# Optimization experiments

Measured on AMD Instinct MI355X. Metric: run time of the kernel, lower is better.

Reference implementation:

```python
import jax, jax.numpy as jnp
import numpy as np

COMMITMENT_COST = 0.25
EMBEDDING_DIM = 64
NUM_EMBEDDINGS = 512
BATCH, SEQ = 64, 4096


def setup_inputs() -> dict:
    key = jax.random.key(0)
    k1, k2, k3 = jax.random.split(key, 3)
    return {
        "inputs": jax.random.normal(k1, (BATCH, SEQ, EMBEDDING_DIM), dtype=jnp.float32),
        "embedding": jax.random.normal(k2, (NUM_EMBEDDINGS, EMBEDDING_DIM), dtype=jnp.float32),
        "ema_cluster_size": jax.random.uniform(k3, (NUM_EMBEDDINGS,), dtype=jnp.float32),
    }


def reference(inputs, embedding, ema_cluster_size):
    # inputs: [B, T, D]; embedding: [K, D]; ema_cluster_size: [K]
    input_shape = inputs.shape
    flat = inputs.reshape(-1, EMBEDDING_DIM)  # [N, D]
    distances = (
        jnp.sum(flat * flat, axis=1, keepdims=True)
        + jnp.sum(embedding * embedding, axis=1)[None, :]
        - 2.0 * (flat @ embedding.T)
    )
    # cluster-size weighting (as in the source module)
    distances = distances * jnp.sqrt(ema_cluster_size)[None, :]
    encoding_indices = jnp.argmin(distances, axis=1)  # [N]
    # one-hot @ codebook == gather
    quantized = embedding[encoding_indices].reshape(input_shape)
    e_latent_loss = jnp.mean((jax.lax.stop_gradient(quantized) - inputs) ** 2)
    loss = COMMITMENT_COST * e_latent_loss
    # straight-through estimator
    quantized_st = inputs + jax.lax.stop_gradient(quantized - inputs)
    return quantized_st, loss, encoding_indices[:, None]
```

## Files before the change

### kernel.cpp

```cpp
#include <hip/hip_runtime.h>
#include <math.h>

#define D 64
#define K 512

typedef __attribute__((ext_vector_type(8))) short short8;
typedef __attribute__((ext_vector_type(4))) float f32x4;

#define WS_E2    256
#define WS_SQ    2304
#define WS_E2SQ  4352
#define WS_TSQ   6400
#define WS_BP    8448
#define WS_WL    139520
#define WS_PART  1188096
#define WS_PART2 1204480

#define KEYMASK 0xFFFFFE00u

__device__ __forceinline__ unsigned short f32_to_bf16_rne(float f)
{
    unsigned int u = __float_as_uint(f);
    unsigned int r = (u + 0x7FFFu + ((u >> 16) & 1u)) >> 16;
    return (unsigned short)r;
}
__device__ __forceinline__ float bf16_to_f32(unsigned short h)
{
    return __uint_as_float(((unsigned int)h) << 16);
}

__device__ __forceinline__ float np_sumsq64(const float* v)
{
#pragma clang fp contract(off)
    float p[64];
#pragma unroll
    for (int i = 0; i < 64; ++i) p[i] = v[i] * v[i];
    float r[8];
#pragma unroll
    for (int j = 0; j < 8; ++j) r[j] = p[j];
#pragma unroll
    for (int b = 8; b < 64; b += 8) {
#pragma unroll
        for (int j = 0; j < 8; ++j) r[j] += p[b + j];
    }
    return ((r[0] + r[1]) + (r[2] + r[3])) + ((r[4] + r[5]) + (r[6] + r[7]));
}

__global__ __launch_bounds__(256) void vq_pack_prep(
    const float* __restrict__ emb,
    const float* __restrict__ cs,
    unsigned short* __restrict__ Bp,
    float* __restrict__ e2,
    float* __restrict__ sq,
    float* __restrict__ e2sq,
    float* __restrict__ tsq,
    int* __restrict__ cnt)
{
    int i = blockIdx.x * blockDim.x + threadIdx.x;
    if (i < 65536) {
        int j    = i & 7;
        int lane = (i >> 3) & 63;
        int kc   = (i >> 9) & 1;
        int ctl  = (i >> 10) & 7;
        int sB   = (i >> 13) & 1;
        int chunk = (i >> 14) & 3;
        int code = chunk * 128 + ctl * 16 + (lane & 15);
        int d    = kc * 32 + (lane >> 4) * 8 + j;
        float v = emb[code * 64 + d];
        unsigned short b0 = f32_to_bf16_rne(v);
        Bp[i] = (sB == 0) ? b0 : f32_to_bf16_rne(v - bf16_to_f32(b0));
    } else if (i < 66048) {
        int k = i - 65536;
        float er[64];
        const float* ek = emb + (size_t)k * D;
#pragma unroll
        for (int d = 0; d < 64; ++d) er[d] = ek[d];
        float e2v = np_sumsq64(er);
        float sqv = (float)sqrt((double)cs[k]);
        e2[k]   = e2v;
        sq[k]   = sqv;
        e2sq[k] = e2v * sqv;
        tsq[k]  = 2.0f * sqv;
    } else if (i == 66048) {
        *cnt = 0;
    }
}

__global__ __launch_bounds__(256) void vq_screen(
    const float* __restrict__ x,
    const float* __restrict__ emb,
    const float* __restrict__ e2sqg,
    const float* __restrict__ tsqg,
    const unsigned short* __restrict__ Bp,
    float* __restrict__ out_q,
    float* __restrict__ out_idx,
    int* __restrict__ wl,
    int* __restrict__ cnt,
    double* __restrict__ partial)
{
    __shared__ unsigned short BpS[16384];
    __shared__ float e2sqs[512];
    __shared__ float tsqs[512];
    __shared__ double ls[4];

    const int wave = threadIdx.x >> 6;
    const int lane = threadIdx.x & 63;
    const int quad = lane >> 4;
    const int n16  = lane & 15;
    const int n0   = blockIdx.x * 128 + wave * 32;

    e2sqs[threadIdx.x]       = e2sqg[threadIdx.x];
    e2sqs[threadIdx.x + 256] = e2sqg[threadIdx.x + 256];
    tsqs[threadIdx.x]        = tsqg[threadIdx.x];
    tsqs[threadIdx.x + 256]  = tsqg[threadIdx.x + 256];

    short8 A0[2][2], A1[2][2];
    float x2h[2][4];
#pragma unroll
    for (int rt = 0; rt < 2; ++rt) {
        float s = 0.0f;
#pragma unroll
        for (int kc = 0; kc < 2; ++kc) {
            const float* src = x + (size_t)(n0 + rt * 16 + n16) * 64
                               + kc * 32 + quad * 8;
            float4 v0 = *(const float4*)(src);
            float4 v1 = *(const float4*)(src + 4);
            float xv[8] = {v0.x, v0.y, v0.z, v0.w, v1.x, v1.y, v1.z, v1.w};
#pragma unroll
            for (int j = 0; j < 8; ++j) {
                float v = xv[j];
                unsigned short b0 = f32_to_bf16_rne(v);
                unsigned short b1 = f32_to_bf16_rne(v - bf16_to_f32(b0));
                A0[rt][kc][j] = (short)b0;
                A1[rt][kc][j] = (short)b1;
                s = fmaf(v, v, s);
            }
        }
        s += __shfl_xor(s, 16, 64);
        s += __shfl_xor(s, 32, 64);
#pragma unroll
        for (int r = 0; r < 4; ++r)
            x2h[rt][r] = 0.5f * __shfl(s, quad * 4 + r, 64);
    }

    unsigned k1[2][4], k2[2][4];
#pragma unroll
    for (int rt = 0; rt < 2; ++rt)
#pragma unroll
        for (int r = 0; r < 4; ++r) { k1[rt][r] = 0xFFFFFFFFu; k2[rt][r] = 0xFFFFFFFFu; }

    for (int chunk = 0; chunk < 4; ++chunk) {
        __syncthreads();
        {
            const float4* src = (const float4*)(Bp + chunk * 16384);
            float4* dst = (float4*)BpS;
#pragma unroll
            for (int it = 0; it < 8; ++it)
                dst[threadIdx.x + it * 256] = src[threadIdx.x + it * 256];
        }
        __syncthreads();

        for (int ctl = 0; ctl < 8; ++ctl) {
            const short8 B00 = *(const short8*)(BpS + (ctl * 2 + 0) * 512 + lane * 8);
            const short8 B01 = *(const short8*)(BpS + (ctl * 2 + 1) * 512 + lane * 8);
            const short8 B10 = *(const short8*)(BpS + ((8 + ctl) * 2 + 0) * 512 + lane * 8);
            const short8 B11 = *(const short8*)(BpS + ((8 + ctl) * 2 + 1) * 512 + lane * 8);

            int c = chunk * 128 + ctl * 16 + n16;
            float e2sqc = e2sqs[c];
            float tsqc  = tsqs[c];

#pragma unroll
            for (int rt = 0; rt < 2; ++rt) {
                f32x4 acc = {0.0f, 0.0f, 0.0f, 0.0f};
                acc = __builtin_amdgcn_mfma_f32_16x16x32_bf16(A0[rt][0], B00, acc, 0, 0, 0);
                acc = __builtin_amdgcn_mfma_f32_16x16x32_bf16(A0[rt][1], B01, acc, 0, 0, 0);
                acc = __builtin_amdgcn_mfma_f32_16x16x32_bf16(A0[rt][0], B10, acc, 0, 0, 0);
                acc = __builtin_amdgcn_mfma_f32_16x16x32_bf16(A0[rt][1], B11, acc, 0, 0, 0);
                acc = __builtin_amdgcn_mfma_f32_16x16x32_bf16(A1[rt][0], B00, acc, 0, 0, 0);
                acc = __builtin_amdgcn_mfma_f32_16x16x32_bf16(A1[rt][1], B01, acc, 0, 0, 0);

#pragma unroll
                for (int r = 0; r < 4; ++r) {
                    float dist = fmaf(x2h[rt][r], tsqc, e2sqc);
                    dist = fmaf(-tsqc, acc[r], dist);
                    dist = fmaxf(dist, 0.0f);
                    unsigned key = (__float_as_uint(dist) & KEYMASK) | (unsigned)c;
                    unsigned a1 = k1[rt][r];
                    unsigned mx = a1 > key ? a1 : key;
                    k1[rt][r] = a1 < key ? a1 : key;
                    k2[rt][r] = k2[rt][r] < mx ? k2[rt][r] : mx;
                }
            }
        }
    }

#pragma unroll
    for (int rt = 0; rt < 2; ++rt)
#pragma unroll
        for (int r = 0; r < 4; ++r) {
            unsigned a1 = k1[rt][r], a2 = k2[rt][r];
#pragma unroll
            for (int w = 1; w < 16; w <<= 1) {
                unsigned o1 = (unsigned)__shfl_xor((int)a1, w, 64);
                unsigned o2 = (unsigned)__shfl_xor((int)a2, w, 64);
                unsigned mx  = a1 > o1 ? a1 : o1;
                a1 = a1 < o1 ? a1 : o1;
                unsigned mn2 = a2 < o2 ? a2 : o2;
                a2 = mn2 < mx ? mn2 : mx;
            }
            k1[rt][r] = a1; k2[rt][r] = a2;
        }

    unsigned pk[2][4];
#pragma unroll
    for (int rt = 0; rt < 2; ++rt)
#pragma unroll
        for (int r = 0; r < 4; ++r) {
            float d1f = __uint_as_float(k1[rt][r] & KEYMASK);
            float d2f = __uint_as_float(k2[rt][r] & KEYMASK);
            int   i1  = (int)(k1[rt][r] & 0x1FFu);
            int   flg = (d2f - d1f) <= (0.01f + 2.0e-4f * d2f);
            pk[rt][r] = (unsigned)i1 | (flg ? 0x8000u : 0u);
            if (n16 == 0) {
                int p = n0 + rt * 16 + quad * 4 + r;
                out_idx[p] = (float)i1;
                if (flg) { int slot = atomicAdd(cnt, 1); wl[slot] = p; }
            }
        }

    int src = (n16 >> 2) * 16 + n16;
    double s = 0.0;
#pragma unroll
    for (int rt = 0; rt < 2; ++rt) {
        unsigned p0 = (unsigned)__shfl((int)pk[rt][0], src, 64);
        unsigned p1 = (unsigned)__shfl((int)pk[rt][1], src, 64);
        unsigned p2 = (unsigned)__shfl((int)pk[rt][2], src, 64);
        unsigned p3 = (unsigned)__shfl((int)pk[rt][3], src, 64);
        int rr = n16 & 3;
        unsigned pm = (rr == 0) ? p0 : (rr == 1) ? p1 : (rr == 2) ? p2 : p3;
        int bim = (int)(pm & 0x1FFu);
        int flg = (int)((pm >> 15) & 1u);
        if (!flg) {
            int prow = n0 + rt * 16 + n16;
#pragma unroll
            for (int kc = 0; kc < 2; ++kc) {
                const float* xs = x   + (size_t)prow * 64 + kc * 32 + quad * 8;
                const float* es = emb + (size_t)bim  * 64 + kc * 32 + quad * 8;
                float4 xv0 = *(const float4*)(xs);
                float4 xv1 = *(const float4*)(xs + 4);
                float4 ev0 = *(const float4*)(es);
                float4 ev1 = *(const float4*)(es + 4);
                float4 o0, o1;
                float t0, t1, t2, t3, t4, t5, t6, t7;
                {
#pragma clang fp contract(off)
                    t0 = ev0.x - xv0.x; o0.x = xv0.x + t0;
                    t1 = ev0.y - xv0.y; o0.y = xv0.y + t1;
                    t2 = ev0.z - xv0.z; o0.z = xv0.z + t2;
                    t3 = ev0.w - xv0.w; o0.w = xv0.w + t3;
                    t4 = ev1.x - xv1.x; o1.x = xv1.x + t4;
                    t5 = ev1.y - xv1.y; o1.y = xv1.y + t5;
                    t6 = ev1.z - xv1.z; o1.z = xv1.z + t6;
                    t7 = ev1.w - xv1.w; o1.w = xv1.w + t7;
                }
                float* od = out_q + (size_t)prow * 64 + kc * 32 + quad * 8;
                *(float4*)(od)     = o0;
                *(float4*)(od + 4) = o1;
                s += (double)t0 * t0 + (double)t1 * t1
                   + (double)t2 * t2 + (double)t3 * t3
                   + (double)t4 * t4 + (double)t5 * t5
                   + (double)t6 * t6 + (double)t7 * t7;
            }
        }
    }

#pragma unroll
    for (int off = 32; off > 0; off >>= 1)
        s += __shfl_down(s, off, 64);
    if (lane == 0) ls[wave] = s;
    __syncthreads();
    if (threadIdx.x == 0)
        partial[blockIdx.x] = ls[0] + ls[1] + ls[2] + ls[3];
}

__global__ __launch_bounds__(256) void vq_exact(
    const float* __restrict__ x,
    const float* __restrict__ emb,
    const float* __restrict__ e2,
    const float* __restrict__ sq,
    const int* __restrict__ wl,
    const int* __restrict__ cnt,
    float* __restrict__ out_idx,
    float* __restrict__ out_q,
    double* __restrict__ partial2)
{
    const int lane = threadIdx.x & 63;
    const int gw   = blockIdx.x * 4 + (threadIdx.x >> 6);
    const int nw   = gridDim.x * 4;
    const int cv   = *cnt;

    for (int w = gw; w < cv; w += nw) {
        int p = wl[w];
        const float* xrow = x + (size_t)p * 64;
        float row[64];
#pragma unroll
        for (int i = 0; i < 16; ++i) {
            float4 v = ((const float4*)xrow)[i];
            row[4 * i + 0] = v.x; row[4 * i + 1] = v.y;
            row[4 * i + 2] = v.z; row[4 * i + 3] = v.w;
        }
        float x2 = np_sumsq64(row);

        float bd = INFINITY;
        int   bc = 0;
        for (int t = 0; t < 8; ++t) {
            int c = t * 64 + lane;
            const float* er = emb + (size_t)c * 64;
            float acc = 0.0f;
#pragma unroll
            for (int d = 0; d < 64; ++d)
                acc = fmaf(row[d], er[d], acc);
            float dist;
            {
#pragma clang fp contract(off)
                dist = ((x2 + e2[c]) - 2.0f * acc) * sq[c];
            }
            if (dist < bd) { bd = dist; bc = c; }
        }
#pragma unroll
        for (int wd = 1; wd < 64; wd <<= 1) {
            float od = __shfl_xor(bd, wd, 64);
            int   oc = __shfl_xor(bc, wd, 64);
            if (od < bd || (od == bd && oc < bc)) { bd = od; bc = oc; }
        }
        if (lane == 0) out_idx[p] = (float)bc;

        float xv = x[(size_t)p * 64 + lane];
        float qv = emb[(size_t)bc * 64 + lane];
        float t, o;
        {
#pragma clang fp contract(off)
            t = qv - xv;
            o = xv + t;
        }
        out_q[(size_t)p * 64 + lane] = o;
        double dd = (double)t * (double)t;
#pragma unroll
        for (int off = 32; off > 0; off >>= 1)
            dd += __shfl_down(dd, off, 64);
        if (lane == 0) partial2[w] = dd;
    }
}

__global__ __launch_bounds__(256) void vq_finalize(
    const double* __restrict__ partial,
    const double* __restrict__ partial2,
    const int* __restrict__ cnt,
    float* __restrict__ loss_out,
    int nblk, double inv_count)
{
    double s = 0.0;
    for (int i = threadIdx.x; i < nblk; i += 256) s += partial[i];
    int cv = *cnt;
    for (int w = threadIdx.x; w < cv; w += 256) s += partial2[w];
#pragma unroll
    for (int off = 32; off > 0; off >>= 1)
        s += __shfl_down(s, off, 64);
    __shared__ double ls[4];
    if ((threadIdx.x & 63) == 0) ls[threadIdx.x >> 6] = s;
    __syncthreads();
    if (threadIdx.x == 0) {
        double total = ls[0] + ls[1] + ls[2] + ls[3];
        loss_out[0] = (float)(0.25 * total * inv_count);
    }
}

extern "C" void kernel_launch(void* const* d_in, const int* in_sizes, int n_in,
                              void* d_out, int out_size, void* d_ws, size_t ws_size,
                              hipStream_t stream)
{
    const float* x   = (const float*)d_in[0];
    const float* emb = (const float*)d_in[1];
    const float* cs  = (const float*)d_in[2];

    const int N = in_sizes[0] / D;

    float* out      = (float*)d_out;
    float* out_q    = out;
    float* out_loss = out + (size_t)N * D;
    float* out_idx  = out_loss + 1;

    char* ws = (char*)d_ws;
    int*            cnt      = (int*)ws;
    float*          e2       = (float*)(ws + WS_E2);
    float*          sq       = (float*)(ws + WS_SQ);
    float*          e2sq     = (float*)(ws + WS_E2SQ);
    float*          tsq      = (float*)(ws + WS_TSQ);
    unsigned short* Bp       = (unsigned short*)(ws + WS_BP);
    int*            wl       = (int*)(ws + WS_WL);
    double*         partial  = (double*)(ws + WS_PART);
    double*         partial2 = (double*)(ws + WS_PART2);

    const int nblk_screen = N / 128;

    vq_pack_prep<<<259, 256, 0, stream>>>(emb, cs, Bp, e2, sq, e2sq, tsq, cnt);
    vq_screen<<<nblk_screen, 256, 0, stream>>>(x, emb, e2sq, tsq, Bp,
                                               out_q, out_idx, wl, cnt, partial);
    vq_exact<<<512, 256, 0, stream>>>(x, emb, e2, sq, wl, cnt,
                                      out_idx, out_q, partial2);
    vq_finalize<<<1, 256, 0, stream>>>(partial, partial2, cnt, out_loss,
                                       nblk_screen, 1.0 / ((double)N * (double)D));
}
```

Measured before the change: 213.4 us.

## Stream packed codebook fragments directly from global memory instead of LDS staging

The screening kernel no longer stages the packed bf16 codebook and the per-code constants in shared memory with block barriers. Each wave now reads its MFMA B fragments and a packed float2 (biased e2*sqrt, 2*sqrt) straight from global memory through the cache, using a re-laid-out fragment order so each tile is contiguous. A small positive bias replaces the fmax clamp, so the key stays non-negative without the extra instruction. This removes the LDS copies and __syncthreads but depends on L1/L2 hits for the 128KB codebook being re-read by every wave, and the bias could shift screening margins.

```diff
diff --git a/kernel.cpp b/kernel.cpp
--- a/kernel.cpp
+++ b/kernel.cpp
@@ -9,14 +9,14 @@
 
 #define WS_E2    256
 #define WS_SQ    2304
-#define WS_E2SQ  4352
-#define WS_TSQ   6400
+#define WS_ETS   4352
 #define WS_BP    8448
 #define WS_WL    139520
 #define WS_PART  1188096
 #define WS_PART2 1204480
 
 #define KEYMASK 0xFFFFFE00u
+#define DIST_BIAS 0.0625f
 
 __device__ __forceinline__ unsigned short f32_to_bf16_rne(float f)
 {
@@ -52,19 +52,18 @@
     unsigned short* __restrict__ Bp,
     float* __restrict__ e2,
     float* __restrict__ sq,
-    float* __restrict__ e2sq,
-    float* __restrict__ tsq,
+    float2* __restrict__ ets,
     int* __restrict__ cnt)
 {
     int i = blockIdx.x * blockDim.x + threadIdx.x;
     if (i < 65536) {
         int j    = i & 7;
         int lane = (i >> 3) & 63;
-        int kc   = (i >> 9) & 1;
-        int ctl  = (i >> 10) & 7;
-        int sB   = (i >> 13) & 1;
-        int chunk = (i >> 14) & 3;
-        int code = chunk * 128 + ctl * 16 + (lane & 15);
+        int frag = (i >> 9) & 3;
+        int t    = (i >> 11) & 31;
+        int kc   = frag & 1;
+        int sB   = frag >> 1;
+        int code = t * 16 + (lane & 15);
         int d    = kc * 32 + (lane >> 4) * 8 + j;
         float v = emb[code * 64 + d];
         unsigned short b0 = f32_to_bf16_rne(v);
@@ -77,10 +76,9 @@
         for (int d = 0; d < 64; ++d) er[d] = ek[d];
         float e2v = np_sumsq64(er);
         float sqv = (float)sqrt((double)cs[k]);
-        e2[k]   = e2v;
-        sq[k]   = sqv;
-        e2sq[k] = e2v * sqv;
-        tsq[k]  = 2.0f * sqv;
+        e2[k] = e2v;
+        sq[k] = sqv;
+        ets[k] = make_float2(e2v * sqv + DIST_BIAS, 2.0f * sqv);
     } else if (i == 66048) {
         *cnt = 0;
     }
@@ -89,8 +87,7 @@
 __global__ __launch_bounds__(256) void vq_screen(
     const float* __restrict__ x,
     const float* __restrict__ emb,
-    const float* __restrict__ e2sqg,
-    const float* __restrict__ tsqg,
+    const float2* __restrict__ ets,
     const unsigned short* __restrict__ Bp,
     float* __restrict__ out_q,
     float* __restrict__ out_idx,
@@ -98,9 +95,6 @@
     int* __restrict__ cnt,
     double* __restrict__ partial)
 {
-    __shared__ unsigned short BpS[16384];
-    __shared__ float e2sqs[512];
-    __shared__ float tsqs[512];
     __shared__ double ls[4];
 
     const int wave = threadIdx.x >> 6;
@@ -108,11 +102,6 @@
     const int quad = lane >> 4;
     const int n16  = lane & 15;
     const int n0   = blockIdx.x * 128 + wave * 32;
-
-    e2sqs[threadIdx.x]       = e2sqg[threadIdx.x];
-    e2sqs[threadIdx.x + 256] = e2sqg[threadIdx.x + 256];
-    tsqs[threadIdx.x]        = tsqg[threadIdx.x];
-    tsqs[threadIdx.x + 256]  = tsqg[threadIdx.x + 256];
 
     short8 A0[2][2], A1[2][2];
     float x2h[2][4];
@@ -149,48 +138,35 @@
 #pragma unroll
         for (int r = 0; r < 4; ++r) { k1[rt][r] = 0xFFFFFFFFu; k2[rt][r] = 0xFFFFFFFFu; }
 
-    for (int chunk = 0; chunk < 4; ++chunk) {
-        __syncthreads();
-        {
-            const float4* src = (const float4*)(Bp + chunk * 16384);
-            float4* dst = (float4*)BpS;
-#pragma unroll
-            for (int it = 0; it < 8; ++it)
-                dst[threadIdx.x + it * 256] = src[threadIdx.x + it * 256];
-        }
-        __syncthreads();
-
-        for (int ctl = 0; ctl < 8; ++ctl) {
-            const short8 B00 = *(const short8*)(BpS + (ctl * 2 + 0) * 512 + lane * 8);
-            const short8 B01 = *(const short8*)(BpS + (ctl * 2 + 1) * 512 + lane * 8);
-            const short8 B10 = *(const short8*)(BpS + ((8 + ctl) * 2 + 0) * 512 + lane * 8);
-            const short8 B11 = *(const short8*)(BpS + ((8 + ctl) * 2 + 1) * 512 + lane * 8);
-
-            int c = chunk * 128 + ctl * 16 + n16;
-            float e2sqc = e2sqs[c];
-            float tsqc  = tsqs[c];
-
-#pragma unroll
-            for (int rt = 0; rt < 2; ++rt) {
-                f32x4 acc = {0.0f, 0.0f, 0.0f, 0.0f};
-                acc = __builtin_amdgcn_mfma_f32_16x16x32_bf16(A0[rt][0], B00, acc, 0, 0, 0);
-                acc = __builtin_amdgcn_mfma_f32_16x16x32_bf16(A0[rt][1], B01, acc, 0, 0, 0);
-                acc = __builtin_amdgcn_mfma_f32_16x16x32_bf16(A0[rt][0], B10, acc, 0, 0, 0);
-                acc = __builtin_amdgcn_mfma_f32_16x16x32_bf16(A0[rt][1], B11, acc, 0, 0, 0);
-                acc = __builtin_amdgcn_mfma_f32_16x16x32_bf16(A1[rt][0], B00, acc, 0, 0, 0);
-                acc = __builtin_amdgcn_mfma_f32_16x16x32_bf16(A1[rt][1], B01, acc, 0, 0, 0);
-
-#pragma unroll
-                for (int r = 0; r < 4; ++r) {
-                    float dist = fmaf(x2h[rt][r], tsqc, e2sqc);
-                    dist = fmaf(-tsqc, acc[r], dist);
-                    dist = fmaxf(dist, 0.0f);
-                    unsigned key = (__float_as_uint(dist) & KEYMASK) | (unsigned)c;
-                    unsigned a1 = k1[rt][r];
-                    unsigned mx = a1 > key ? a1 : key;
-                    k1[rt][r] = a1 < key ? a1 : key;
-                    k2[rt][r] = k2[rt][r] < mx ? k2[rt][r] : mx;
-                }
+#pragma unroll 2
+    for (int t = 0; t < 32; ++t) {
+        const unsigned short* bp = Bp + t * 2048 + lane * 8;
+        const short8 B00 = *(const short8*)(bp);
+        const short8 B01 = *(const short8*)(bp + 512);
+        const short8 B10 = *(const short8*)(bp + 1024);
+        const short8 B11 = *(const short8*)(bp + 1536);
+        float2 et = ets[t * 16 + n16];
+        unsigned cbits = (unsigned)(t * 16 + n16);
+
+#pragma unroll
+        for (int rt = 0; rt < 2; ++rt) {
+            f32x4 acc = {0.0f, 0.0f, 0.0f, 0.0f};
+            acc = __builtin_amdgcn_mfma_f32_16x16x32_bf16(A0[rt][0], B00, acc, 0, 0, 0);
+            acc = __builtin_amdgcn_mfma_f32_16x16x32_bf16(A0[rt][1], B01, acc, 0, 0, 0);
+            acc = __builtin_amdgcn_mfma_f32_16x16x32_bf16(A0[rt][0], B10, acc, 0, 0, 0);
+            acc = __builtin_amdgcn_mfma_f32_16x16x32_bf16(A0[rt][1], B11, acc, 0, 0, 0);
+            acc = __builtin_amdgcn_mfma_f32_16x16x32_bf16(A1[rt][0], B00, acc, 0, 0, 0);
+            acc = __builtin_amdgcn_mfma_f32_16x16x32_bf16(A1[rt][1], B01, acc, 0, 0, 0);
+
+#pragma unroll
+            for (int r = 0; r < 4; ++r) {
+                float dist = fmaf(x2h[rt][r], et.y, et.x);
+                dist = fmaf(-et.y, acc[r], dist);
+                unsigned key = (__float_as_uint(dist) & KEYMASK) | cbits;
+                unsigned a1 = k1[rt][r];
+                unsigned mx = a1 > key ? a1 : key;
+                k1[rt][r] = a1 < key ? a1 : key;
+                k2[rt][r] = k2[rt][r] < mx ? k2[rt][r] : mx;
             }
         }
     }
@@ -395,8 +371,7 @@
     int*            cnt      = (int*)ws;
     float*          e2       = (float*)(ws + WS_E2);
     float*          sq       = (float*)(ws + WS_SQ);
-    float*          e2sq     = (float*)(ws + WS_E2SQ);
-    float*          tsq      = (float*)(ws + WS_TSQ);
+    float2*         ets      = (float2*)(ws + WS_ETS);
     unsigned short* Bp       = (unsigned short*)(ws + WS_BP);
     int*            wl       = (int*)(ws + WS_WL);
     double*         partial  = (double*)(ws + WS_PART);
@@ -404,8 +379,8 @@
 
     const int nblk_screen = N / 128;
 
-    vq_pack_prep<<<259, 256, 0, stream>>>(emb, cs, Bp, e2, sq, e2sq, tsq, cnt);
-    vq_screen<<<nblk_screen, 256, 0, stream>>>(x, emb, e2sq, tsq, Bp,
+    vq_pack_prep<<<259, 256, 0, stream>>>(emb, cs, Bp, e2, sq, ets, cnt);
+    vq_screen<<<nblk_screen, 256, 0, stream>>>(x, emb, ets, Bp,
                                                out_q, out_idx, wl, cnt, partial);
     vq_exact<<<512, 256, 0, stream>>>(x, emb, e2, sq, wl, cnt,
                                       out_idx, out_q, partial2);
```

Measured after the change: 214.6 us. About the same (+0.5%).
